# Kernel optimization log

Hardware: AMD Instinct MI355X
Metric: run time of the kernel (lower is better)

The kernel has to match this reference:

```python
import jax, jax.numpy as jnp
import numpy as np


def fps(xyz, npoint):
    # xyz: [B, N, 3] -> idx [B, npoint]; iterative farthest point sampling (start at index 0)
    B, N, _ = xyz.shape
    dist0 = jnp.full((B, N), 1e10, xyz.dtype)
    far0 = jnp.zeros((B,), jnp.int32)
    def body(carry, _):
        dist, far = carry
        centroid = jnp.take_along_axis(xyz, far[:, None, None], axis=1)  # [B,1,3]
        d = jnp.sum((xyz - centroid) ** 2, axis=-1)                      # [B,N]
        dist = jnp.minimum(dist, d)
        return (dist, jnp.argmax(dist, axis=-1).astype(jnp.int32)), far
    _, idx = jax.lax.scan(body, (dist0, far0), None, length=npoint)
    return idx.T  # [B, npoint]


def ball_query(radius, nsample, xyz, new_xyz):
    # xyz [B,N,3], new_xyz [B,S,3] -> idx [B,S,nsample]
    B, S, _ = new_xyz.shape
    N = xyz.shape[1]
    sqr = jnp.sum((new_xyz[:, :, None, :] - xyz[:, None, :, :]) ** 2, axis=-1)  # [B,S,N]
    idx = jnp.broadcast_to(jnp.arange(N, dtype=jnp.int32), (B, S, N))
    idx = jnp.where(sqr > radius * radius, N, idx)
    idx = jnp.sort(idx, axis=-1)[:, :, :nsample]
    first = idx[:, :, :1]
    return jnp.where(idx == N, first, idx)


def index_points(points, idx):
    # points [B,N,C], idx [B,...] int -> [B,...,C]
    B = points.shape[0]
    out = jnp.take_along_axis(points, idx.reshape(B, -1, 1), axis=1)
    return out.reshape(idx.shape + (points.shape[-1],))


def set_abstraction(xyz, points, npoint, radius, nsample, ws, bs):
    fidx = fps(xyz, npoint)
    new_xyz = index_points(xyz, fidx)                       # [B,S,3]
    gidx = ball_query(radius, nsample, xyz, new_xyz)        # [B,S,ns]
    grouped = index_points(xyz, gidx) - new_xyz[:, :, None, :]  # centered neighbors
    if points is not None:
        grouped = jnp.concatenate([grouped, index_points(points, gidx)], axis=-1)
    x = grouped                                             # [B,S,ns,Cin]
    for w, b in zip(ws, bs):  # shared 1x1-conv MLP (eval-mode BN folded into w,b) + ReLU
        x = jax.nn.relu(jnp.einsum('bsnc,oc->bsno', x, w) + b)
    return new_xyz, jnp.max(x, axis=2)                      # max-pool over neighbors


def sa_group_all(xyz, points, ws, bs):
    x = jnp.concatenate([xyz, points], axis=-1)             # [B,N,3+C]
    for w, b in zip(ws, bs):
        x = jax.nn.relu(jnp.einsum('bnc,oc->bno', x, w) + b)
    return jnp.max(x, axis=1)                               # [B,1024]


def setup_inputs() -> dict:
    key = jax.random.key(0)
    ks = iter(jax.random.split(key, 64))
    def w(shape):
        return jax.random.normal(next(ks), shape, jnp.float32) * 0.02
    d = {"xyz": jax.random.normal(next(ks), (32, 3, 4096), jnp.float32)}
    mlps = {"s1": [(64, 3), (64, 64), (128, 64)],
            "s2": [(128, 131), (128, 128), (256, 128)],
            "s3": [(256, 259), (512, 256), (1024, 512)]}
    for name, layers in mlps.items():
        for i, (o, c) in enumerate(layers):
            d[name + "w" + str(i)] = w((o, c))
            d[name + "b" + str(i)] = jnp.zeros((o,), jnp.float32)
    for name, (o, c) in {"f1": (512, 1024), "f2": (256, 512), "f3": (6, 256)}.items():
        d[name + "w"] = w((o, c))
        d[name + "b"] = jnp.zeros((o,), jnp.float32)
    return d


def reference(xyz, s1w0, s1b0, s1w1, s1b1, s1w2, s1b2,
              s2w0, s2b0, s2w1, s2b1, s2w2, s2b2,
              s3w0, s3b0, s3w1, s3b1, s3w2, s3b2,
              f1w, f1b, f2w, f2b, f3w, f3b):
    pts = jnp.transpose(xyz, (0, 2, 1))  # [B,N,3]
    l1x, l1p = set_abstraction(pts, None, 512, 0.2, 32, [s1w0, s1w1, s1w2], [s1b0, s1b1, s1b2])
    l2x, l2p = set_abstraction(l1x, l1p, 128, 0.4, 64, [s2w0, s2w1, s2w2], [s2b0, s2b1, s2b2])
    feat = sa_group_all(l2x, l2p, [s3w0, s3w1, s3w2], [s3b0, s3b1, s3b2])  # [B,1024]
    x = jax.nn.relu(feat @ f1w.T + f1b)   # fc1 + (folded BN) + ReLU; dropout=identity (eval)
    x = jax.nn.relu(x @ f2w.T + f2b)
    return x @ f3w.T + f3b                # [B,6] value head (softmax=False)
```

## Files before the change

### kernel.cpp

```cpp
#include <hip/hip_runtime.h>
#include <hip/hip_bf16.h>
#include <hip/hip_cooperative_groups.h>

namespace cg = cooperative_groups;


typedef __attribute__((ext_vector_type(8))) short short8;
typedef __attribute__((ext_vector_type(4))) float f32x4;
union SV8 { short8 v; ushort u[8]; };

__device__ __forceinline__ ushort f2bf(float x) {
    unsigned u = __float_as_uint(x);
    unsigned r = (u + 0x7fffu + ((u >> 16) & 1u)) >> 16;
    return (ushort)r;
}

template<int CTRL>
__device__ __forceinline__ unsigned long long dpp_mov_u64(unsigned long long x) {
    const int lo = (int)(unsigned)(x & 0xffffffffull);
    const int hi = (int)(unsigned)(x >> 32);
    const int nlo = __builtin_amdgcn_update_dpp(lo, lo, CTRL, 0xf, 0xf, false);
    const int nhi = __builtin_amdgcn_update_dpp(hi, hi, CTRL, 0xf, 0xf, false);
    return ((unsigned long long)(unsigned)nhi << 32) | (unsigned)nlo;
}

__device__ __forceinline__ unsigned long long wave_max_u64(unsigned long long x) {
    unsigned long long y;
    y = dpp_mov_u64<0x111>(x); if (y > x) x = y;
    y = dpp_mov_u64<0x112>(x); if (y > x) x = y;
    y = dpp_mov_u64<0x114>(x); if (y > x) x = y;
    y = dpp_mov_u64<0x118>(x); if (y > x) x = y;
    y = dpp_mov_u64<0x142>(x); if (y > x) x = y;
    y = dpp_mov_u64<0x143>(x); if (y > x) x = y;
    return x;
}

template<int N, int S, int NT, bool CHW>
__device__ __forceinline__ void fps_body(const float* __restrict__ xyz,
                                         float* __restrict__ new_xyz,
                                         int b, int t, char* smem) {
    constexpr int P  = N / NT;
    constexpr int NW = NT / 64;
    float4* sxyz = (float4*)smem;
    unsigned long long* rv = (unsigned long long*)(smem + (size_t)N * 16);
    int* sfar = (int*)(smem + (size_t)N * 16 + 2 * NW * 8);
    float px[P], py[P], pz[P], dist[P];
    unsigned idc[P];
    if (CHW) {
        const float* base = xyz + (size_t)b * 3 * N;
        #pragma unroll
        for (int p = 0; p < P; ++p) {
            const int i = p * NT + t;
            px[p] = base[i]; py[p] = base[N + i]; pz[p] = base[2 * N + i];
            sxyz[i] = make_float4(px[p], py[p], pz[p], 0.0f);
        }
    } else {
        const float* base = xyz + (size_t)b * N * 3;
        #pragma unroll
        for (int p = 0; p < P; ++p) {
            const int i = p * NT + t;
            px[p] = base[i*3]; py[p] = base[i*3+1]; pz[p] = base[i*3+2];
            sxyz[i] = make_float4(px[p], py[p], pz[p], 0.0f);
        }
    }
    #pragma unroll
    for (int p = 0; p < P; ++p) { dist[p] = 1e10f; idc[p] = (unsigned)(N - 1 - (p * NT + t)); }
    __syncthreads();
    int far = 0;
    for (int j = 0; j < S; ++j) {
        if (t == 0) sfar[j] = far;
        const float4 cen = sxyz[far];
        unsigned long long pk[P];
        #pragma unroll
        for (int p = 0; p < P; ++p) {
            const float dx = px[p] - cen.x, dy = py[p] - cen.y, dz = pz[p] - cen.z;
            const float d = __fadd_rn(__fadd_rn(__fmul_rn(dx, dx), __fmul_rn(dy, dy)), __fmul_rn(dz, dz));
            const float nd = fminf(dist[p], d);
            dist[p] = nd;
            pk[p] = ((unsigned long long)__float_as_uint(nd) << 32) | idc[p];
        }
        #pragma unroll
        for (int s = P / 2; s > 0; s >>= 1)
            #pragma unroll
            for (int k = 0; k < s; ++k)
                if (pk[k + s] > pk[k]) pk[k] = pk[k + s];
        unsigned long long best = wave_max_u64(pk[0]);
        if constexpr (NW > 1) {
            const int sl = (j & 1) * NW;
            if ((t & 63) == 63) rv[sl + (t >> 6)] = best;
            __syncthreads();
            unsigned long long bb = rv[sl];
            #pragma unroll
            for (int w = 1; w < NW; ++w) { const unsigned long long v = rv[sl + w]; if (v > bb) bb = v; }
            far = N - 1 - (int)(bb & 0xffffffffull);
        } else {
            far = N - 1 - __builtin_amdgcn_readlane((int)(best & 0xffffffffull), 63);
        }
    }
    __syncthreads();
    float* out = new_xyz + (size_t)b * S * 3;
    for (int i = t; i < S; i += NT) {
        const float4 c = sxyz[sfar[i]];
        out[i*3+0] = c.x; out[i*3+1] = c.y; out[i*3+2] = c.z;
    }
}

__device__ __forceinline__ void packg(const float* __restrict__ src,
                                      ushort* __restrict__ dh,
                                      int Ktot, int otiles, int cofs, int idx) {
    const int j = idx & 7, lane = (idx >> 3) & 63;
    const int ot = (idx >> 9) % otiles;
    const int ks = idx / (512 * otiles);
    const int m = lane & 15, q = lane >> 4;
    const int o = ot * 16 + m, c = cofs + ks * 32 + q * 8 + j;
    const float v = (c < Ktot) ? src[(size_t)o * Ktot + c] : 0.0f;
    dh[idx] = f2bf(v);
}

__global__ __launch_bounds__(256)
void fps1_prep_kernel(const float* __restrict__ xyz, float* __restrict__ l1xyz,
                 const float* s1w0, const float* s1b0, float4* Wc1,
                 const float* s1w1, ushort* M1W1h,
                 const float* s1w2, ushort* M1W2h,
                 const float* s3w0, ushort* S3W0h,
                 const float* s3w1, ushort* S3W1h,
                 const float* s3w2, ushort* S3W2h,
                 const float* s2w0, const float* s2b0, float4* Wc0,
                 ushort* W0h,
                 const float* s2w1, ushort* W1h,
                 const float* s2w2, ushort* W2h) {
    __shared__ __align__(16) char smem[4096 * 16 + 64 + 512 * 4];
    if (blockIdx.x < 32) {
        fps_body<4096, 512, 256, true>(xyz, l1xyz, blockIdx.x, threadIdx.x, smem);
        return;
    }
    int i = (blockIdx.x - 32) * 256 + threadIdx.x;
    if (i < 64)     { Wc1[i] = make_float4(s1w0[i*3], s1w0[i*3+1], s1w0[i*3+2], s1b0[i]); return; }  i -= 64;
    if (i < 4096)   { packg(s1w1, M1W1h,  64,  4, 0, i); return; }   i -= 4096;
    if (i < 8192)   { packg(s1w2, M1W2h,  64,  8, 0, i); return; }   i -= 8192;
    if (i < 73728)  { packg(s3w0, S3W0h, 259, 16, 0, i); return; }   i -= 73728;
    if (i < 131072) { packg(s3w1, S3W1h, 256, 32, 0, i); return; }   i -= 131072;
    if (i < 524288) { packg(s3w2, S3W2h, 512, 64, 0, i); return; }   i -= 524288;
    if (i < 16384)  { packg(s2w0, W0h, 131,  8, 3, i); return; }     i -= 16384;
    if (i < 16384)  { packg(s2w1, W1h, 128,  8, 0, i); return; }     i -= 16384;
    if (i < 32768)  { packg(s2w2, W2h, 128, 16, 0, i); return; }     i -= 32768;
    if (i < 128) {
        Wc0[i] = make_float4(s2w0[(size_t)i*131+0], s2w0[(size_t)i*131+1],
                             s2w0[(size_t)i*131+2], s2b0[i]);
    }
}

template<int N, int NS, bool CHW, int NT>
__global__ __launch_bounds__(NT)
void bq_kernel(float r2, const float* __restrict__ xyz, const float* __restrict__ cen,
               int* __restrict__ gidx, int S) {
    constexpr int WPB = NT / 64;
    __shared__ __align__(16) float4 sp[N];
    const int t = threadIdx.x, lane = t & 63, w = t >> 6;
    const int cen0 = blockIdx.x * WPB;
    const int b = cen0 / S;
    if (CHW) {
        const float* base = xyz + (size_t)b * 3 * N;
        for (int i = t; i < N; i += NT)
            sp[i] = make_float4(base[i], base[N + i], base[2 * N + i], 0.0f);
    } else {
        const float* base = xyz + (size_t)b * N * 3;
        for (int i = t; i < N; i += NT)
            sp[i] = make_float4(base[i*3], base[i*3+1], base[i*3+2], 0.0f);
    }
    __syncthreads();
    const int wid = cen0 + w;
    const float cx = cen[(size_t)wid*3+0], cy = cen[(size_t)wid*3+1], cz = cen[(size_t)wid*3+2];
    int* out = gidx + (size_t)wid * NS;
    int cnt = 0, first = -1;
    for (int b0 = 0; b0 < N; b0 += 64) {
        const float4 p = sp[b0 + lane];
        const float dx = p.x - cx, dy = p.y - cy, dz = p.z - cz;
        const float d = __fadd_rn(__fadd_rn(__fmul_rn(dx, dx), __fmul_rn(dy, dy)), __fmul_rn(dz, dz));
        const bool in = (d <= r2);
        const unsigned long long m = __ballot(in);
        if (first < 0 && m != 0ull) first = b0 + __ffsll((unsigned long long)m) - 1;
        const int pos = cnt + (int)__popcll(m & ((1ull << lane) - 1ull));
        if (in && pos < NS) out[pos] = b0 + lane;
        cnt += (int)__popcll(m);
        if (cnt >= NS) break;
    }
    if (cnt < NS)
        for (int k = cnt + lane; k < NS; k += 64) out[k] = first;
}

__global__ __launch_bounds__(256)
void mlp1_kernel(const float* __restrict__ xyz, const float* __restrict__ l1xyz,
                 float* __restrict__ l2xyz,
                 const int* __restrict__ gidx, const float4* __restrict__ Wc1,
                 const ushort* __restrict__ W1h, const float* __restrict__ b1,
                 const ushort* __restrict__ W2h, const float* __restrict__ b2,
                 float* __restrict__ l1p) {
    __shared__ __align__(16) char smem[64 * 68 * 4 * 2];
    float* bufA = (float*)smem;
    float* bufB = (float*)(smem + 64 * 68 * 4);
    const int t = threadIdx.x, b = blockIdx.y;
    if (blockIdx.x == 256) {
        fps_body<512, 128, 256, false>(l1xyz, l2xyz, b, t, smem);
        return;
    }
    const int s0 = blockIdx.x * 2;
    {
        const int n = t >> 2, c = t & 3;
        const int s = s0 + (n >> 5);
        const int gi = gidx[((size_t)b * 512 + s) * 32 + (n & 31)];
        float v = 0.0f;
        if (c < 3) v = xyz[(size_t)b * 3 * 4096 + c * 4096 + gi] - l1xyz[((size_t)b * 512 + s) * 3 + c];
        bufB[n * 4 + c] = v;
    }
    __syncthreads();
    {
        const int o = t & 63, ng = t >> 6;
        const float4 wc = Wc1[o];
        #pragma unroll
        for (int r = 0; r < 16; ++r) {
            const int n = ng * 16 + r;
            const float z = wc.w + wc.x * bufB[n*4] + wc.y * bufB[n*4+1] + wc.z * bufB[n*4+2];
            bufA[n * 68 + o] = fmaxf(z, 0.0f);
        }
    }
    const int lane = t & 63, wv = t >> 6;
    const int m = lane & 15, q = lane >> 4;
    const int rowA = wv * 16 + m;
    f32x4 acc1[4];
    #pragma unroll
    for (int ot = 0; ot < 4; ++ot)
        #pragma unroll
        for (int r = 0; r < 4; ++r) acc1[ot][r] = 0.0f;
    #pragma unroll
    for (int ks = 0; ks < 2; ++ks) {
        float xv[8];
        *(float4*)&xv[0] = *(const float4*)&bufA[rowA * 68 + ks * 32 + q * 8];
        *(float4*)&xv[4] = *(const float4*)&bufA[rowA * 68 + ks * 32 + q * 8 + 4];
        SV8 ah;
        #pragma unroll
        for (int j = 0; j < 8; ++j) ah.u[j] = f2bf(xv[j]);
        #pragma unroll
        for (int ot = 0; ot < 4; ++ot) {
            SV8 bh;
            bh.v = *(const short8*)(W1h + (size_t)((ks * 4 + ot) * 64 + lane) * 8);
            acc1[ot] = __builtin_amdgcn_mfma_f32_16x16x32_bf16(ah.v, bh.v, acc1[ot], 0, 0, 0);
        }
    }
    #pragma unroll
    for (int ot = 0; ot < 4; ++ot) {
        const float bb = b1[ot * 16 + m];
        #pragma unroll
        for (int r = 0; r < 4; ++r)
            bufB[(wv * 16 + q * 4 + r) * 68 + ot * 16 + m] = fmaxf(acc1[ot][r] + bb, 0.0f);
    }
    f32x4 acc2[8];
    #pragma unroll
    for (int ot = 0; ot < 8; ++ot)
        #pragma unroll
        for (int r = 0; r < 4; ++r) acc2[ot][r] = 0.0f;
    #pragma unroll
    for (int ks = 0; ks < 2; ++ks) {
        float xv[8];
        *(float4*)&xv[0] = *(const float4*)&bufB[rowA * 68 + ks * 32 + q * 8];
        *(float4*)&xv[4] = *(const float4*)&bufB[rowA * 68 + ks * 32 + q * 8 + 4];
        SV8 ah;
        #pragma unroll
        for (int j = 0; j < 8; ++j) ah.u[j] = f2bf(xv[j]);
        #pragma unroll
        for (int ot = 0; ot < 8; ++ot) {
            SV8 bh;
            bh.v = *(const short8*)(W2h + (size_t)((ks * 8 + ot) * 64 + lane) * 8);
            acc2[ot] = __builtin_amdgcn_mfma_f32_16x16x32_bf16(ah.v, bh.v, acc2[ot], 0, 0, 0);
        }
    }
    __syncthreads();
    #pragma unroll
    for (int ot = 0; ot < 8; ++ot) {
        const float bb = b2[ot * 16 + m];
        float mx = 0.0f;
        #pragma unroll
        for (int r = 0; r < 4; ++r) mx = fmaxf(mx, acc2[ot][r] + bb);
        bufA[(wv * 4 + q) * 128 + ot * 16 + m] = mx;
    }
    __syncthreads();
    {
        const int half = t >> 7, o = t & 127;
        float v = bufA[(half * 8) * 128 + o];
        #pragma unroll
        for (int rr = 1; rr < 8; ++rr) v = fmaxf(v, bufA[(half * 8 + rr) * 128 + o]);
        l1p[((size_t)b * 512 + s0 + half) * 128 + o] = v;
    }
}

__global__ __launch_bounds__(256)
void mlp2_kernel(const float* __restrict__ l1xyz, const float* __restrict__ l1p,
                 const float* __restrict__ l2xyz,
                 const ushort* __restrict__ W0h, const float4* __restrict__ Wc0,
                 const ushort* __restrict__ W1h, const float* __restrict__ b1,
                 const ushort* __restrict__ W2h, const float* __restrict__ b2,
                 float* __restrict__ X3) {
    __shared__ __align__(16) float Abuf[64 * 132];
    __shared__ __align__(16) float Bbuf[64 * 132];
    __shared__ int sg[64];
    __shared__ __align__(16) float4 sp4[512];
    const int t = threadIdx.x, bs = blockIdx.x, b = bs >> 7;
    {
        const float* base = l1xyz + (size_t)b * 512 * 3;
        for (int i = t; i < 512; i += 256)
            sp4[i] = make_float4(base[i*3], base[i*3+1], base[i*3+2], 0.0f);
    }
    if (t < 3)  X3[(size_t)bs * 288 + t] = l2xyz[(size_t)bs * 3 + t];
    if (t >= 64 && t < 93) X3[(size_t)bs * 288 + 259 + (t - 64)] = 0.0f;
    __syncthreads();
    if (t < 64) {
        const float r2 = (float)(0.4 * 0.4);
        const float cx = l2xyz[(size_t)bs*3+0], cy = l2xyz[(size_t)bs*3+1], cz = l2xyz[(size_t)bs*3+2];
        int cnt = 0, first = -1;
        for (int b0 = 0; b0 < 512; b0 += 64) {
            const float4 p = sp4[b0 + t];
            const float dx = p.x - cx, dy = p.y - cy, dz = p.z - cz;
            const float d = __fadd_rn(__fadd_rn(__fmul_rn(dx, dx), __fmul_rn(dy, dy)), __fmul_rn(dz, dz));
            const bool in = (d <= r2);
            const unsigned long long mm = __ballot(in);
            if (first < 0 && mm != 0ull) first = b0 + __ffsll((unsigned long long)mm) - 1;
            const int pos = cnt + (int)__popcll(mm & ((1ull << t) - 1ull));
            if (in && pos < 64) sg[pos] = b0 + t;
            cnt += (int)__popcll(mm);
            if (cnt >= 64) break;
        }
        if (cnt < 64)
            for (int k = cnt + t; k < 64; k += 64) sg[k] = first;
    }
    __syncthreads();
    for (int i = t; i < 64 * 32; i += 256) {
        const int n = i >> 5, cc = i & 31;
        *(float4*)&Abuf[n * 132 + cc * 4] =
            *(const float4*)&l1p[((size_t)b * 512 + sg[n]) * 128 + cc * 4];
    }
    if (t < 192) {
        const int n = t / 3, c = t % 3;
        const float4 pp = sp4[sg[n]];
        const float pc = (c == 0) ? pp.x : (c == 1) ? pp.y : pp.z;
        Abuf[n * 132 + 128 + c] = pc - l2xyz[(size_t)bs * 3 + c];
    }
    __syncthreads();
    const int lane = t & 63, wv = t >> 6;
    const int m = lane & 15, q = lane >> 4;
    const int rowA = wv * 16 + m;

    f32x4 acc0[8];
    #pragma unroll
    for (int ot = 0; ot < 8; ++ot)
        #pragma unroll
        for (int r = 0; r < 4; ++r) acc0[ot][r] = 0.0f;
    #pragma unroll
    for (int ks = 0; ks < 4; ++ks) {
        float xv[8];
        *(float4*)&xv[0] = *(const float4*)&Abuf[rowA * 132 + ks * 32 + q * 8];
        *(float4*)&xv[4] = *(const float4*)&Abuf[rowA * 132 + ks * 32 + q * 8 + 4];
        SV8 ah;
        #pragma unroll
        for (int j = 0; j < 8; ++j) ah.u[j] = f2bf(xv[j]);
        #pragma unroll
        for (int ot = 0; ot < 8; ++ot) {
            SV8 bh;
            bh.v = *(const short8*)(W0h + (size_t)((ks * 8 + ot) * 64 + lane) * 8);
            acc0[ot] = __builtin_amdgcn_mfma_f32_16x16x32_bf16(ah.v, bh.v, acc0[ot], 0, 0, 0);
        }
    }
    float crd[4][3];
    #pragma unroll
    for (int r = 0; r < 4; ++r) {
        const int n = wv * 16 + q * 4 + r;
        crd[r][0] = Abuf[n * 132 + 128];
        crd[r][1] = Abuf[n * 132 + 129];
        crd[r][2] = Abuf[n * 132 + 130];
    }
    #pragma unroll
    for (int ot = 0; ot < 8; ++ot) {
        const float4 wc = Wc0[ot * 16 + m];
        #pragma unroll
        for (int r = 0; r < 4; ++r) {
            const float v = acc0[ot][r] + wc.w + wc.x * crd[r][0] + wc.y * crd[r][1] + wc.z * crd[r][2];
            Bbuf[(wv * 16 + q * 4 + r) * 132 + ot * 16 + m] = fmaxf(v, 0.0f);
        }
    }
    __syncthreads();

    f32x4 acc1[8];
    #pragma unroll
    for (int ot = 0; ot < 8; ++ot)
        #pragma unroll
        for (int r = 0; r < 4; ++r) acc1[ot][r] = 0.0f;
    #pragma unroll
    for (int ks = 0; ks < 4; ++ks) {
        float xv[8];
        *(float4*)&xv[0] = *(const float4*)&Bbuf[rowA * 132 + ks * 32 + q * 8];
        *(float4*)&xv[4] = *(const float4*)&Bbuf[rowA * 132 + ks * 32 + q * 8 + 4];
        SV8 ah;
        #pragma unroll
        for (int j = 0; j < 8; ++j) ah.u[j] = f2bf(xv[j]);
        #pragma unroll
        for (int ot = 0; ot < 8; ++ot) {
            SV8 bh;
            bh.v = *(const short8*)(W1h + (size_t)((ks * 8 + ot) * 64 + lane) * 8);
            acc1[ot] = __builtin_amdgcn_mfma_f32_16x16x32_bf16(ah.v, bh.v, acc1[ot], 0, 0, 0);
        }
    }
    __syncthreads();
    #pragma unroll
    for (int ot = 0; ot < 8; ++ot) {
        const float bb = b1[ot * 16 + m];
        #pragma unroll
        for (int r = 0; r < 4; ++r)
            Abuf[(wv * 16 + q * 4 + r) * 132 + ot * 16 + m] = fmaxf(acc1[ot][r] + bb, 0.0f);
    }
    __syncthreads();

    f32x4 acc2[16];
    #pragma unroll
    for (int ot = 0; ot < 16; ++ot)
        #pragma unroll
        for (int r = 0; r < 4; ++r) acc2[ot][r] = 0.0f;
    #pragma unroll
    for (int ks = 0; ks < 4; ++ks) {
        float xv[8];
        *(float4*)&xv[0] = *(const float4*)&Abuf[rowA * 132 + ks * 32 + q * 8];
        *(float4*)&xv[4] = *(const float4*)&Abuf[rowA * 132 + ks * 32 + q * 8 + 4];
        SV8 ah;
        #pragma unroll
        for (int j = 0; j < 8; ++j) ah.u[j] = f2bf(xv[j]);
        #pragma unroll
        for (int ot = 0; ot < 16; ++ot) {
            SV8 bh;
            bh.v = *(const short8*)(W2h + (size_t)((ks * 16 + ot) * 64 + lane) * 8);
            acc2[ot] = __builtin_amdgcn_mfma_f32_16x16x32_bf16(ah.v, bh.v, acc2[ot], 0, 0, 0);
        }
    }
    __syncthreads();
    #pragma unroll
    for (int ot = 0; ot < 16; ++ot) {
        const float bb = b2[ot * 16 + m];
        float mx = 0.0f;
        #pragma unroll
        for (int r = 0; r < 4; ++r) mx = fmaxf(mx, acc2[ot][r] + bb);
        Bbuf[(wv * 4 + q) * 256 + ot * 16 + m] = mx;
    }
    __syncthreads();
    {
        float v = Bbuf[t];
        #pragma unroll
        for (int rr = 1; rr < 16; ++rr) v = fmaxf(v, Bbuf[rr * 256 + t]);
        X3[(size_t)bs * 288 + 3 + t] = v;
    }
}

__device__ __forceinline__ void gemm_tile4(const float* __restrict__ A, int AS,
                                           const ushort* __restrict__ Wh,
                                           const float* __restrict__ bias,
                                           float* __restrict__ C, int O,
                                           int KSTEPS, int rt, int bo,
                                           int lane, int wv, int m, int q) {
    const int rowA = rt * 64 + wv * 16 + m;
    const int OT = O >> 4;
    f32x4 acc[4];
    #pragma unroll
    for (int ot = 0; ot < 4; ++ot)
        #pragma unroll
        for (int r = 0; r < 4; ++r) acc[ot][r] = 0.0f;
    for (int ks = 0; ks < KSTEPS; ++ks) {
        float xv[8];
        *(float4*)&xv[0] = *(const float4*)&A[(size_t)rowA * AS + ks * 32 + q * 8];
        *(float4*)&xv[4] = *(const float4*)&A[(size_t)rowA * AS + ks * 32 + q * 8 + 4];
        SV8 ah;
        #pragma unroll
        for (int j = 0; j < 8; ++j) ah.u[j] = f2bf(xv[j]);
        #pragma unroll
        for (int ot = 0; ot < 4; ++ot) {
            const size_t wb = (size_t)((ks * OT + bo * 4 + ot) * 64 + lane) * 8;
            SV8 bh;
            bh.v = *(const short8*)(Wh + wb);
            acc[ot] = __builtin_amdgcn_mfma_f32_16x16x32_bf16(ah.v, bh.v, acc[ot], 0, 0, 0);
        }
    }
    #pragma unroll
    for (int ot = 0; ot < 4; ++ot) {
        const int col = (bo * 4 + ot) * 16 + m;
        const float bb = bias[col];
        #pragma unroll
        for (int r = 0; r < 4; ++r) {
            const int row = rt * 64 + wv * 16 + q * 4 + r;
            C[(size_t)row * O + col] = fmaxf(acc[ot][r] + bb, 0.0f);
        }
    }
}

__global__ __launch_bounds__(256)
void tail_coop_kernel(const float* __restrict__ X3,
                      const ushort* __restrict__ W0h, const float* __restrict__ b0,
                      const ushort* __restrict__ W1h, const float* __restrict__ b1,
                      const ushort* __restrict__ W2h, const float* __restrict__ b2,
                      float* __restrict__ Y1, float* __restrict__ Y2,
                      float* __restrict__ P3,
                      const float* __restrict__ f1w, const float* __restrict__ f1b,
                      const float* __restrict__ f2w, const float* __restrict__ f2b,
                      const float* __restrict__ f3w, const float* __restrict__ f3b,
                      float* __restrict__ out) {
    cg::grid_group grid = cg::this_grid();
    __shared__ float part[16][64];
    __shared__ __align__(16) float xb[1024];
    __shared__ __align__(16) float h1b[512];
    __shared__ __align__(16) float h2b[256];
    const int t = threadIdx.x, lane = t & 63, wv = t >> 6;
    const int m = lane & 15, q = lane >> 4;
    const int bid = blockIdx.x;
    const int rt = bid >> 2, bq4 = bid & 3;

    gemm_tile4(X3, 288, W0h, b0, Y1, 256, 9, rt, bq4, lane, wv, m, q);
    grid.sync();

    #pragma unroll
    for (int j = 0; j < 2; ++j)
        gemm_tile4(Y1, 256, W1h, b1, Y2, 512, 8, rt, bq4 * 2 + j, lane, wv, m, q);
    grid.sync();

    for (int j = 0; j < 4; ++j) {
        const int bo = bq4 * 4 + j;
        f32x4 acc[4];
        #pragma unroll
        for (int ot = 0; ot < 4; ++ot)
            #pragma unroll
            for (int r = 0; r < 4; ++r) acc[ot][r] = 0.0f;
        const int rowA = rt * 64 + wv * 16 + m;
        for (int ks = 0; ks < 16; ++ks) {
            float xv[8];
            *(float4*)&xv[0] = *(const float4*)&Y2[(size_t)rowA * 512 + ks * 32 + q * 8];
            *(float4*)&xv[4] = *(const float4*)&Y2[(size_t)rowA * 512 + ks * 32 + q * 8 + 4];
            SV8 ah;
            #pragma unroll
            for (int jj = 0; jj < 8; ++jj) ah.u[jj] = f2bf(xv[jj]);
            #pragma unroll
            for (int ot = 0; ot < 4; ++ot) {
                const size_t wb = (size_t)((ks * 64 + bo * 4 + ot) * 64 + lane) * 8;
                SV8 bh;
                bh.v = *(const short8*)(W2h + wb);
                acc[ot] = __builtin_amdgcn_mfma_f32_16x16x32_bf16(ah.v, bh.v, acc[ot], 0, 0, 0);
            }
        }
        #pragma unroll
        for (int ot = 0; ot < 4; ++ot) {
            const float bb = b2[(bo * 4 + ot) * 16 + m];
            float mx = 0.0f;
            #pragma unroll
            for (int r = 0; r < 4; ++r) mx = fmaxf(mx, acc[ot][r] + bb);
            part[wv * 4 + q][ot * 16 + m] = mx;
        }
        __syncthreads();
        for (int o = t; o < 64; o += 256) {
            float v = part[0][o];
            #pragma unroll
            for (int rr = 1; rr < 16; ++rr) v = fmaxf(v, part[rr][o]);
            P3[(size_t)rt * 1024 + bo * 64 + o] = v;
        }
        __syncthreads();
    }
    grid.sync();

    if (bid >= 32) return;
    const int b = bid;
    for (int i = t; i < 1024; i += 256)
        xb[i] = fmaxf(P3[(size_t)(2*b)*1024 + i], P3[(size_t)(2*b+1)*1024 + i]);
    __syncthreads();
    #pragma unroll
    for (int oo = 0; oo < 2; ++oo) {
        const int o = t + oo * 256;
        const float4* wr = (const float4*)(f1w + (size_t)o * 1024);
        float s0 = 0, s1 = 0, s2 = 0, s3 = 0;
        for (int c = 0; c < 256; ++c) {
            const float4 w4 = wr[c];
            const float4 xv = *(const float4*)&xb[c * 4];
            s0 += w4.x * xv.x; s1 += w4.y * xv.y; s2 += w4.z * xv.z; s3 += w4.w * xv.w;
        }
        h1b[o] = fmaxf(f1b[o] + ((s0 + s1) + (s2 + s3)), 0.0f);
    }
    __syncthreads();
    {
        const float4* wr = (const float4*)(f2w + (size_t)t * 512);
        float s0 = 0, s1 = 0, s2 = 0, s3 = 0;
        for (int c = 0; c < 128; ++c) {
            const float4 w4 = wr[c];
            const float4 xv = *(const float4*)&h1b[c * 4];
            s0 += w4.x * xv.x; s1 += w4.y * xv.y; s2 += w4.z * xv.z; s3 += w4.w * xv.w;
        }
        h2b[t] = fmaxf(f2b[t] + ((s0 + s1) + (s2 + s3)), 0.0f);
    }
    __syncthreads();
    if (t < 6) {
        const float4* wr = (const float4*)(f3w + (size_t)t * 256);
        float s0 = 0, s1 = 0, s2 = 0, s3 = 0;
        for (int c = 0; c < 64; ++c) {
            const float4 w4 = wr[c];
            const float4 xv = *(const float4*)&h2b[c * 4];
            s0 += w4.x * xv.x; s1 += w4.y * xv.y; s2 += w4.z * xv.z; s3 += w4.w * xv.w;
        }
        out[b * 6 + t] = f3b[t] + ((s0 + s1) + (s2 + s3));
    }
}

extern "C" void kernel_launch(void* const* d_in, const int* in_sizes, int n_in,
                              void* d_out, int out_size, void* d_ws, size_t ws_size,
                              hipStream_t stream) {
    const float* xyz  = (const float*)d_in[0];
    const float* s1w0 = (const float*)d_in[1];  const float* s1b0 = (const float*)d_in[2];
    const float* s1w1 = (const float*)d_in[3];  const float* s1b1 = (const float*)d_in[4];
    const float* s1w2 = (const float*)d_in[5];  const float* s1b2 = (const float*)d_in[6];
    const float* s2w0 = (const float*)d_in[7];  const float* s2b0 = (const float*)d_in[8];
    const float* s2w1 = (const float*)d_in[9];  const float* s2b1 = (const float*)d_in[10];
    const float* s2w2 = (const float*)d_in[11]; const float* s2b2 = (const float*)d_in[12];
    const float* s3w0 = (const float*)d_in[13]; const float* s3b0 = (const float*)d_in[14];
    const float* s3w1 = (const float*)d_in[15]; const float* s3b1 = (const float*)d_in[16];
    const float* s3w2 = (const float*)d_in[17]; const float* s3b2 = (const float*)d_in[18];
    const float* f1w  = (const float*)d_in[19]; const float* f1b  = (const float*)d_in[20];
    const float* f2w  = (const float*)d_in[21]; const float* f2b  = (const float*)d_in[22];
    const float* f3w  = (const float*)d_in[23]; const float* f3b  = (const float*)d_in[24];

    char* ws = (char*)d_ws;
    float* l1_xyz = (float*)(ws + 0);
    int*   gidx1  = (int*)  (ws + 196608);
    float* l1p    = (float*)(ws + 2293760);
    float* l2_xyz = (float*)(ws + 10682368);
    float* X3p    = (float*)(ws + 11780096);
    const size_t PK = 16498688;
    float4* Wc1   = (float4*)(ws + PK + 0);
    ushort* M1W1h = (ushort*)(ws + PK + 1024);
    ushort* M1W2h = (ushort*)(ws + PK + 17408);
    ushort* W0h   = (ushort*)(ws + PK + 50176);
    ushort* W1h   = (ushort*)(ws + PK + 115712);
    ushort* W2h   = (ushort*)(ws + PK + 181248);
    float4* Wc0   = (float4*)(ws + PK + 312320);
    ushort* S3W0h = (ushort*)(ws + PK + 314368);
    ushort* S3W1h = (ushort*)(ws + PK + 609280);
    ushort* S3W2h = (ushort*)(ws + PK + 1133568);
    float* Y1   = (float*)(ws + 19729408);
    float* Y2   = (float*)(ws + 23923712);
    float* P3   = (float*)(ws + 32312320);

    fps1_prep_kernel<<<3186, 256, 0, stream>>>(xyz, l1_xyz,
        s1w0, s1b0, Wc1, s1w1, M1W1h, s1w2, M1W2h,
        s3w0, S3W0h, s3w1, S3W1h, s3w2, S3W2h,
        s2w0, s2b0, Wc0, W0h, s2w1, W1h, s2w2, W2h);
    bq_kernel<4096, 32, true, 1024><<<1024, 1024, 0, stream>>>(
        (float)(0.2 * 0.2), xyz, l1_xyz, gidx1, 512);
    {
        dim3 g(257, 32);
        mlp1_kernel<<<g, 256, 0, stream>>>(xyz, l1_xyz, l2_xyz, gidx1,
            Wc1, M1W1h, s1b1, M1W2h, s1b2, l1p);
    }

    mlp2_kernel<<<4096, 256, 0, stream>>>(l1_xyz, l1p, l2_xyz,
        W0h, Wc0, W1h, s2b1, W2h, s2b2, X3p);

    {
        float* dout = (float*)d_out;
        void* args[] = {
            (void*)&X3p, (void*)&S3W0h, (void*)&s3b0,
            (void*)&S3W1h, (void*)&s3b1, (void*)&S3W2h, (void*)&s3b2,
            (void*)&Y1, (void*)&Y2, (void*)&P3,
            (void*)&f1w, (void*)&f1b, (void*)&f2w, (void*)&f2b,
            (void*)&f3w, (void*)&f3b, (void*)&dout
        };
        hipLaunchCooperativeKernel((const void*)tail_coop_kernel,
                                   dim3(256), dim3(256), args, 0, stream);
    }
    (void)in_sizes; (void)n_in; (void)out_size; (void)ws_size;
}
```

Measured before the change: 902.3 us.

## Replace cooperative grid syncs with per-row-tile atomic flags in tail kernel

The tail stage no longer launches cooperatively with three grid-wide syncs. It now runs as a regular 1024-block kernel in which each 64-row tile signals its completion through global atomic counters, and only the dependent blocks spin-wait on them. The counters are zeroed by mlp2_kernel. The mlp1 grid is transposed so the FPS blocks (blockIdx.y==0) are dispatched first, and the FPS loop raises wave priority with s_setprio. Together these aim to remove the cooperative launch overhead and global barriers and to start the serial FPS work early. The cost is the risk of spin-wait deadlock if waiting blocks take up slots that producer blocks need, plus memory-fence subtleties.

Result: slower. 1.359 ms (+50.6%).

```diff
diff --git a/kernel.cpp b/kernel.cpp
--- a/kernel.cpp
+++ b/kernel.cpp
@@ -1,8 +1,5 @@
 #include <hip/hip_runtime.h>
 #include <hip/hip_bf16.h>
-#include <hip/hip_cooperative_groups.h>
-
-namespace cg = cooperative_groups;
 
 
 typedef __attribute__((ext_vector_type(8))) short short8;
@@ -66,6 +63,7 @@
     #pragma unroll
     for (int p = 0; p < P; ++p) { dist[p] = 1e10f; idc[p] = (unsigned)(N - 1 - (p * NT + t)); }
     __syncthreads();
+    __builtin_amdgcn_s_setprio(1);
     int far = 0;
     for (int j = 0; j < S; ++j) {
         if (t == 0) sfar[j] = far;
@@ -97,6 +95,7 @@
             far = N - 1 - __builtin_amdgcn_readlane((int)(best & 0xffffffffull), 63);
         }
     }
+    __builtin_amdgcn_s_setprio(0);
     __syncthreads();
     float* out = new_xyz + (size_t)b * S * 3;
     for (int i = t; i < S; i += NT) {
@@ -199,12 +198,12 @@
     __shared__ __align__(16) char smem[64 * 68 * 4 * 2];
     float* bufA = (float*)smem;
     float* bufB = (float*)(smem + 64 * 68 * 4);
-    const int t = threadIdx.x, b = blockIdx.y;
-    if (blockIdx.x == 256) {
+    const int t = threadIdx.x, b = blockIdx.x;
+    if (blockIdx.y == 0) {
         fps_body<512, 128, 256, false>(l1xyz, l2xyz, b, t, smem);
         return;
     }
-    const int s0 = blockIdx.x * 2;
+    const int s0 = (blockIdx.y - 1) * 2;
     {
         const int n = t >> 2, c = t & 3;
         const int s = s0 + (n >> 5);
@@ -299,12 +298,13 @@
                  const ushort* __restrict__ W0h, const float4* __restrict__ Wc0,
                  const ushort* __restrict__ W1h, const float* __restrict__ b1,
                  const ushort* __restrict__ W2h, const float* __restrict__ b2,
-                 float* __restrict__ X3) {
+                 float* __restrict__ X3, int* __restrict__ flg) {
     __shared__ __align__(16) float Abuf[64 * 132];
     __shared__ __align__(16) float Bbuf[64 * 132];
     __shared__ int sg[64];
     __shared__ __align__(16) float4 sp4[512];
     const int t = threadIdx.x, bs = blockIdx.x, b = bs >> 7;
+    if (bs == 0 && t < 192) flg[t] = 0;
     {
         const float* base = l1xyz + (size_t)b * 512 * 3;
         for (int i = t; i < 512; i += 256)
@@ -456,11 +456,12 @@
     }
 }
 
-__device__ __forceinline__ void gemm_tile4(const float* __restrict__ A, int AS,
+template<int KSTEPS>
+__device__ __forceinline__ void gemm4_relu(const float* __restrict__ A, int AS,
                                            const ushort* __restrict__ Wh,
                                            const float* __restrict__ bias,
                                            float* __restrict__ C, int O,
-                                           int KSTEPS, int rt, int bo,
+                                           int rt, int bo,
                                            int lane, int wv, int m, int q) {
     const int rowA = rt * 64 + wv * 16 + m;
     const int OT = O >> 4;
@@ -496,43 +497,53 @@
     }
 }
 
-__global__ __launch_bounds__(256)
-void tail_coop_kernel(const float* __restrict__ X3,
-                      const ushort* __restrict__ W0h, const float* __restrict__ b0,
-                      const ushort* __restrict__ W1h, const float* __restrict__ b1,
-                      const ushort* __restrict__ W2h, const float* __restrict__ b2,
-                      float* __restrict__ Y1, float* __restrict__ Y2,
-                      float* __restrict__ P3,
-                      const float* __restrict__ f1w, const float* __restrict__ f1b,
-                      const float* __restrict__ f2w, const float* __restrict__ f2b,
-                      const float* __restrict__ f3w, const float* __restrict__ f3b,
-                      float* __restrict__ out) {
-    cg::grid_group grid = cg::this_grid();
+__global__ __launch_bounds__(256, 4)
+void tail_kernel(const float* __restrict__ X3,
+                 const ushort* __restrict__ W0h, const float* __restrict__ b0,
+                 const ushort* __restrict__ W1h, const float* __restrict__ b1,
+                 const ushort* __restrict__ W2h, const float* __restrict__ b2,
+                 float* __restrict__ Y1, float* __restrict__ Y2,
+                 float* __restrict__ P3,
+                 const float* __restrict__ f1w, const float* __restrict__ f1b,
+                 const float* __restrict__ f2w, const float* __restrict__ f2b,
+                 const float* __restrict__ f3w, const float* __restrict__ f3b,
+                 float* __restrict__ out, int* __restrict__ flg) {
     __shared__ float part[16][64];
     __shared__ __align__(16) float xb[1024];
     __shared__ __align__(16) float h1b[512];
     __shared__ __align__(16) float h2b[256];
+    int* F1 = flg; int* F2 = flg + 64; int* F3 = flg + 128;
     const int t = threadIdx.x, lane = t & 63, wv = t >> 6;
     const int m = lane & 15, q = lane >> 4;
-    const int bid = blockIdx.x;
-    const int rt = bid >> 2, bq4 = bid & 3;
-
-    gemm_tile4(X3, 288, W0h, b0, Y1, 256, 9, rt, bq4, lane, wv, m, q);
-    grid.sync();
-
-    #pragma unroll
-    for (int j = 0; j < 2; ++j)
-        gemm_tile4(Y1, 256, W1h, b1, Y2, 512, 8, rt, bq4 * 2 + j, lane, wv, m, q);
-    grid.sync();
-
-    for (int j = 0; j < 4; ++j) {
-        const int bo = bq4 * 4 + j;
+    const int bid = blockIdx.x, rt = bid >> 4, j = bid & 15;
+
+    if (j < 4) {
+        gemm4_relu<9>(X3, 288, W0h, b0, Y1, 256, rt, j, lane, wv, m, q);
+        __threadfence();
+        __syncthreads();
+        if (t == 0) atomicAdd(&F1[rt], 1);
+    }
+    if (t == 0) { while (atomicAdd(&F1[rt], 0) < 4) __builtin_amdgcn_s_sleep(2); }
+    __syncthreads();
+    __threadfence();
+
+    if (j < 8) {
+        gemm4_relu<8>(Y1, 256, W1h, b1, Y2, 512, rt, j, lane, wv, m, q);
+        __threadfence();
+        __syncthreads();
+        if (t == 0) atomicAdd(&F2[rt], 1);
+    }
+    if (t == 0) { while (atomicAdd(&F2[rt], 0) < 8) __builtin_amdgcn_s_sleep(2); }
+    __syncthreads();
+    __threadfence();
+
+    {
+        const int rowA = rt * 64 + wv * 16 + m;
         f32x4 acc[4];
         #pragma unroll
         for (int ot = 0; ot < 4; ++ot)
             #pragma unroll
             for (int r = 0; r < 4; ++r) acc[ot][r] = 0.0f;
-        const int rowA = rt * 64 + wv * 16 + m;
         for (int ks = 0; ks < 16; ++ks) {
             float xv[8];
             *(float4*)&xv[0] = *(const float4*)&Y2[(size_t)rowA * 512 + ks * 32 + q * 8];
@@ -542,7 +553,7 @@
             for (int jj = 0; jj < 8; ++jj) ah.u[jj] = f2bf(xv[jj]);
             #pragma unroll
             for (int ot = 0; ot < 4; ++ot) {
-                const size_t wb = (size_t)((ks * 64 + bo * 4 + ot) * 64 + lane) * 8;
+                const size_t wb = (size_t)((ks * 64 + j * 4 + ot) * 64 + lane) * 8;
                 SV8 bh;
                 bh.v = *(const short8*)(W2h + wb);
                 acc[ot] = __builtin_amdgcn_mfma_f32_16x16x32_bf16(ah.v, bh.v, acc[ot], 0, 0, 0);
@@ -550,7 +561,7 @@
         }
         #pragma unroll
         for (int ot = 0; ot < 4; ++ot) {
-            const float bb = b2[(bo * 4 + ot) * 16 + m];
+            const float bb = b2[(j * 4 + ot) * 16 + m];
             float mx = 0.0f;
             #pragma unroll
             for (int r = 0; r < 4; ++r) mx = fmaxf(mx, acc[ot][r] + bb);
@@ -561,14 +572,21 @@
             float v = part[0][o];
             #pragma unroll
             for (int rr = 1; rr < 16; ++rr) v = fmaxf(v, part[rr][o]);
-            P3[(size_t)rt * 1024 + bo * 64 + o] = v;
-        }
-        __syncthreads();
-    }
-    grid.sync();
-
-    if (bid >= 32) return;
-    const int b = bid;
+            P3[(size_t)rt * 1024 + j * 64 + o] = v;
+        }
+    }
+    __threadfence();
+    __syncthreads();
+    if (t == 0) atomicAdd(&F3[rt], 1);
+
+    if (j != 15 || (rt & 1) == 0) return;
+    const int b = rt >> 1;
+    if (t == 0) {
+        while (atomicAdd(&F3[rt - 1], 0) < 16) __builtin_amdgcn_s_sleep(2);
+        while (atomicAdd(&F3[rt], 0) < 16) __builtin_amdgcn_s_sleep(2);
+    }
+    __syncthreads();
+    __threadfence();
     for (int i = t; i < 1024; i += 256)
         xb[i] = fmaxf(P3[(size_t)(2*b)*1024 + i], P3[(size_t)(2*b+1)*1024 + i]);
     __syncthreads();
@@ -630,6 +648,7 @@
     int*   gidx1  = (int*)  (ws + 196608);
     float* l1p    = (float*)(ws + 2293760);
     float* l2_xyz = (float*)(ws + 10682368);
+    int*   flg    = (int*)  (ws + 10731520);
     float* X3p    = (float*)(ws + 11780096);
     const size_t PK = 16498688;
     float4* Wc1   = (float4*)(ws + PK + 0);
@@ -653,25 +672,16 @@
     bq_kernel<4096, 32, true, 1024><<<1024, 1024, 0, stream>>>(
         (float)(0.2 * 0.2), xyz, l1_xyz, gidx1, 512);
     {
-        dim3 g(257, 32);
+        dim3 g(32, 257);
         mlp1_kernel<<<g, 256, 0, stream>>>(xyz, l1_xyz, l2_xyz, gidx1,
             Wc1, M1W1h, s1b1, M1W2h, s1b2, l1p);
     }
 
     mlp2_kernel<<<4096, 256, 0, stream>>>(l1_xyz, l1p, l2_xyz,
-        W0h, Wc0, W1h, s2b1, W2h, s2b2, X3p);
-
-    {
-        float* dout = (float*)d_out;
-        void* args[] = {
-            (void*)&X3p, (void*)&S3W0h, (void*)&s3b0,
-            (void*)&S3W1h, (void*)&s3b1, (void*)&S3W2h, (void*)&s3b2,
-            (void*)&Y1, (void*)&Y2, (void*)&P3,
-            (void*)&f1w, (void*)&f1b, (void*)&f2w, (void*)&f2b,
-            (void*)&f3w, (void*)&f3b, (void*)&dout
-        };
-        hipLaunchCooperativeKernel((const void*)tail_coop_kernel,
-                                   dim3(256), dim3(256), args, 0, stream);
-    }
+        W0h, Wc0, W1h, s2b1, W2h, s2b2, X3p, flg);
+
+    tail_kernel<<<1024, 256, 0, stream>>>(X3p, S3W0h, s3b0, S3W1h, s3b1,
+        S3W2h, s3b2, Y1, Y2, P3, f1w, f1b, f2w, f2b, f3w, f3b,
+        (float*)d_out, flg);
     (void)in_sizes; (void)n_in; (void)out_size; (void)ws_size;
 }
```
